# Kernel optimization log

Measured on AMD Instinct MI355X. Metric: run time of the kernel, lower is better.

## Reference

```python
import jax, jax.numpy as jnp
import numpy as np

P, T, S, D, V, H, FF, L, BLOCK = 4096, 1024, 4, 2048, 32000, 8, 8192, 2, 16
DH = D // H


def _rms(x, g):
    return x * g * jax.lax.rsqrt(jnp.mean(x * x, axis=-1, keepdims=True) + 1e-6)


def _attn(xq, xkv, mask, Wqkv, Wo):
    q = (xq @ Wqkv[:, :D]).reshape(-1, H, DH)
    k = (xkv @ Wqkv[:, D:2 * D]).reshape(-1, H, DH)
    v = (xkv @ Wqkv[:, 2 * D:]).reshape(-1, H, DH)
    s = jnp.einsum('qhd,khd->hqk', q, k) / jnp.asarray(np.sqrt(DH), q.dtype)
    s = jnp.where(mask[None], s, -1e30)
    p = jax.nn.softmax(s, axis=-1)
    o = jnp.einsum('hqk,khd->qhd', p, v).reshape(-1, D)
    return o @ Wo


def _forward(prefix_input_ids, prefix_batch_ids, prefix_position_ids, input_ids,
             batch_ids, position_ids, tail_gather_indices, labels, num_items_in_batch,
             Wt_embed, Wt_qkv, Wt_o, Wt_m1, Wt_m2, gt_ln1, gt_ln2, gt_lnf,
             Wd_embed, Wd_qkv, Wd_o, Wd_m1, Wd_m2, gd_ln1, gd_ln2, gd_lnf):
    # ---- target causal prefill (frozen, torch.no_grad): batch-aware prefix-causal mask ----
    mask_p = (prefix_batch_ids[:, None] == prefix_batch_ids[None, :]) & \
             (prefix_position_ids[:, None] >= prefix_position_ids[None, :])  # [P,P]
    x = Wt_embed[prefix_input_ids]
    for l in range(L):
        xn = _rms(x, gt_ln1[l])
        x = x + _attn(xn, xn, mask_p, Wt_qkv[l], Wt_o[l])
        x = x + jax.nn.gelu(_rms(x, gt_ln2[l]) @ Wt_m1[l]) @ Wt_m2[l]
    hidden = jax.lax.stop_gradient(x)  # extract_context_feature -> last hidden state [P,D]
    logits_t = jax.lax.stop_gradient(_rms(x, gt_lnf) @ Wt_embed.T)  # [P,V]
    # ---- draft block-sparse mask (flex_mask_mod) ----
    full_b = jnp.concatenate([prefix_batch_ids, batch_ids])
    full_p = jnp.concatenate([prefix_position_ids, position_ids])
    qidx = jnp.arange(T)
    kvidx = jnp.arange(P + T)
    qblk = qidx // BLOCK
    anchor_p = position_ids[qblk * BLOCK]  # position of block anchor token [T]
    batch_match = batch_ids[:, None] == full_b[None, :]
    prefix_vis = (kvidx < P)[None, :] & (anchor_p[:, None] > full_p[None, :])
    tail_blk_match = qblk[:, None] == ((kvidx - P) // BLOCK)[None, :]
    mask_d = batch_match & (prefix_vis | tail_blk_match)  # [T, P+T]
    # ---- draft forward: q = tail noise tokens, kv = [prefix hidden ; tail embeds] ----
    xq = Wd_embed[input_ids]
    xkv = jnp.concatenate([hidden, xq], axis=0)
    y = xq + _attn(_rms(xq, gd_ln1), _rms(xkv, gd_ln1), mask_d, Wd_qkv, Wd_o)
    y = y + jax.nn.gelu(_rms(y, gd_ln2) @ Wd_m1) @ Wd_m2
    logits_d = _rms(y, gd_lnf) @ Wd_embed.T  # [T,V]
    # ---- KD loss: forward KL(teacher || student), masked where labels == -100 ----
    teacher = logits_t[tail_gather_indices]
    lpt = jax.nn.log_softmax(teacher, axis=-1)
    lps = jax.nn.log_softmax(logits_d, axis=-1)
    kl = jnp.sum(jnp.exp(lpt) * (lpt - lps), axis=-1)  # [T]
    loss = jnp.where(labels != -100, kl, 0.0).sum() / num_items_in_batch
    return loss


def setup_inputs() -> dict:
    key = jax.random.key(0)
    ks = jax.random.split(key, 16)
    seq, tail = P // S, T // S  # 1024 prefix tokens / 256 tail tokens per sequence
    prefix_batch_ids = jnp.asarray(np.repeat(np.arange(S), seq), jnp.int32)
    prefix_position_ids = jnp.asarray(np.tile(np.arange(seq), S), jnp.int32)
    batch_ids = jnp.asarray(np.repeat(np.arange(S), tail), jnp.int32)
    position_ids = jnp.asarray(np.tile(seq - tail + np.arange(tail), S), jnp.int32)
    tail_gather_indices = jnp.asarray(
        np.repeat(np.arange(S), tail) * seq + np.tile(seq - tail - 1 + np.arange(tail), S), jnp.int32)
    labels = jax.random.randint(ks[0], (T,), 0, V, dtype=jnp.int32).at[::17].set(-100)
    w = lambda k, shape: (0.02 * jax.random.normal(k, shape)).astype(jnp.float32)
    return {
        'prefix_input_ids': jax.random.randint(ks[1], (P,), 0, V, dtype=jnp.int32),
        'prefix_batch_ids': prefix_batch_ids,
        'prefix_position_ids': prefix_position_ids,
        'input_ids': jax.random.randint(ks[2], (T,), 0, V, dtype=jnp.int32),
        'batch_ids': batch_ids,
        'position_ids': position_ids,
        'tail_gather_indices': tail_gather_indices,
        'labels': labels,
        'num_items_in_batch': 4,
        'Wt_embed': w(ks[3], (V, D)),
        'Wt_qkv': w(ks[4], (L, D, 3 * D)),
        'Wt_o': w(ks[5], (L, D, D)),
        'Wt_m1': w(ks[6], (L, D, FF)),
        'Wt_m2': w(ks[7], (L, FF, D)),
        'gt_ln1': jnp.ones((L, D), jnp.float32),
        'gt_ln2': jnp.ones((L, D), jnp.float32),
        'gt_lnf': jnp.ones((D,), jnp.float32),
        'Wd_embed': w(ks[8], (V, D)),
        'Wd_qkv': w(ks[9], (D, 3 * D)),
        'Wd_o': w(ks[10], (D, D)),
        'Wd_m1': w(ks[11], (D, FF)),
        'Wd_m2': w(ks[12], (FF, D)),
        'gd_ln1': jnp.ones((D,), jnp.float32),
        'gd_ln2': jnp.ones((D,), jnp.float32),
        'gd_lnf': jnp.ones((D,), jnp.float32),
    }


def reference(prefix_input_ids, prefix_batch_ids, prefix_position_ids, input_ids,
              batch_ids, position_ids, tail_gather_indices, labels, num_items_in_batch,
              Wt_embed, Wt_qkv, Wt_o, Wt_m1, Wt_m2, gt_ln1, gt_ln2, gt_lnf,
              Wd_embed, Wd_qkv, Wd_o, Wd_m1, Wd_m2, gd_ln1, gd_ln2, gd_lnf):
    return _forward(prefix_input_ids, prefix_batch_ids, prefix_position_ids, input_ids,
                    batch_ids, position_ids, tail_gather_indices, labels, num_items_in_batch,
                    Wt_embed, Wt_qkv, Wt_o, Wt_m1, Wt_m2, gt_ln1, gt_ln2, gt_lnf,
                    Wd_embed, Wd_qkv, Wd_o, Wd_m1, Wd_m2, gd_ln1, gd_ln2, gd_lnf)
```

## Files before the change

kernel.cpp:

```cpp
#include <hip/hip_runtime.h>
#include <math.h>

#define P_TOK 4096
#define T_TOK 1024
#define KV_TOK 5120
#define DIM 2048
#define VOCAB 32000
#define NHEAD 8
#define DHEAD 256
#define FFDIM 8192
#define NLAYER 2

using f32x4  = __attribute__((ext_vector_type(4))) float;
using bf16x4 = __attribute__((ext_vector_type(4))) __bf16;
using bf16x8 = __attribute__((ext_vector_type(8))) __bf16;

typedef const __attribute__((address_space(1))) void* gp1_t;
typedef __attribute__((address_space(3))) void* lp3_t;

__device__ __forceinline__ void gload16(const void* g, void* l) {
  __builtin_amdgcn_global_load_lds((gp1_t)g, (lp3_t)l, 16, 0, 0);
}

__device__ __forceinline__ unsigned pack_bf2(float a, float b) {
  union { __bf16 h[2]; unsigned u; } x;
  x.h[0] = (__bf16)a; x.h[1] = (__bf16)b; return x.u;
}

__device__ __forceinline__ float gelu_tanh(float u) {
  const float k2 = 1.5957691216057308f * (u + 0.044715f * u * u * u);
  return u / (1.0f + __expf(-k2));
}

template<typename CT, bool ACCUM, int EPI>
__global__ __launch_bounds__(256) void gemm_bt(
    const __bf16* __restrict__ A, const __bf16* __restrict__ B, CT* __restrict__ C,
    int M, int N, int K, int lda, int ldb, int ldc)
{
  __shared__ __align__(16) __bf16 As[2][128][64];
  __shared__ __align__(16) __bf16 Bs[2][128][64];
  const int tid = threadIdx.x;
  const int lane = tid & 63, wave = tid >> 6;

  int bx = blockIdx.x, by = blockIdx.y;
  {
    const int gx = gridDim.x, gy = gridDim.y;
    const int nwg = gx * gy;
    if ((nwg & 7) == 0) {
      const int lin = bx * gy + by;
      const int cpx = nwg >> 3;
      const int swz = (lin & 7) * cpx + (lin >> 3);
      bx = swz / gy; by = swz % gy;
    }
  }
  const int bm = by << 7, bn = bx << 7;

  const int fr = lane & 15, fq = lane >> 4;
  const int wm = (wave >> 1) << 6, wn = (wave & 1) << 6;
  const int l8 = lane >> 3;
  const int c8 = ((lane & 7) ^ l8) << 3;
  const int sw = fr & 7;

  const __bf16* ga[4]; const __bf16* gb[4];
  char* la[4]; char* lb[4];
#pragma unroll
  for (int i = 0; i < 4; ++i) {
    const int c = (wave << 2) + i;
    const int row = (c << 3) + l8;
    ga[i] = A + (size_t)(bm + row) * lda + c8;
    gb[i] = B + (size_t)(bn + row) * ldb + c8;
    la[i] = (char*)(&As[0][0][0]) + (c << 10);
    lb[i] = (char*)(&Bs[0][0][0]) + (c << 10);
  }
  f32x4 acc[4][4] = {};

  const int nk = K >> 6;

#pragma unroll
  for (int i = 0; i < 4; ++i) { gload16(ga[i], la[i]); gload16(gb[i], lb[i]); }
#pragma unroll
  for (int i = 0; i < 4; ++i) { gload16(ga[i] + 64, la[i] + 16384); gload16(gb[i] + 64, lb[i] + 16384); }

  auto step = [&](const int buf, const int t) {
    if (t + 2 < nk) asm volatile("s_waitcnt vmcnt(8)" ::: "memory");
    else            asm volatile("s_waitcnt vmcnt(0)" ::: "memory");
    asm volatile("s_barrier" ::: "memory");
    bf16x8 a[2][4], b[2][4];
#pragma unroll
    for (int ks = 0; ks < 2; ++ks) {
      const int ce = (((ks << 2) + fq) ^ sw) << 3;
#pragma unroll
      for (int i = 0; i < 4; ++i) {
        a[ks][i] = *reinterpret_cast<const bf16x8*>(&As[buf][wm + (i << 4) + fr][ce]);
        b[ks][i] = *reinterpret_cast<const bf16x8*>(&Bs[buf][wn + (i << 4) + fr][ce]);
      }
    }
    asm volatile("s_waitcnt lgkmcnt(0)" ::: "memory");
    asm volatile("s_barrier" ::: "memory");
    if (t + 2 < nk) {
      const int k2 = (t + 2) << 6;
      const int lo = buf << 14;
#pragma unroll
      for (int i = 0; i < 4; ++i) {
        gload16(ga[i] + k2, la[i] + lo);
        gload16(gb[i] + k2, lb[i] + lo);
      }
    }
    __builtin_amdgcn_sched_barrier(0);
#pragma unroll
    for (int ks = 0; ks < 2; ++ks)
#pragma unroll
      for (int mi = 0; mi < 4; ++mi)
#pragma unroll
        for (int ni = 0; ni < 4; ++ni)
          acc[mi][ni] = __builtin_amdgcn_mfma_f32_16x16x32_bf16(a[ks][mi], b[ks][ni], acc[mi][ni], 0, 0, 0);
  };
  for (int t = 0; t < nk; t += 2) { step(0, t); step(1, t + 1); }

#pragma unroll
  for (int mi = 0; mi < 4; ++mi) {
#pragma unroll
    for (int r = 0; r < 4; ++r) {
      const size_t rowi = (size_t)(bm + wm + (mi << 4) + (fq << 2) + r);
      CT* Crow = C + rowi * ldc + bn + wn + fr;
#pragma unroll
      for (int ni = 0; ni < 4; ++ni) {
        float v = acc[mi][ni][r];
        if (EPI == 1) v = gelu_tanh(v);
        if (ACCUM) Crow[ni << 4] += (CT)v;
        else       Crow[ni << 4] = (CT)v;
      }
    }
  }
}

template<int MODE>
__global__ __launch_bounds__(256, 2) void flash_attn(
    const __bf16* __restrict__ Q, int ldq,
    const __bf16* __restrict__ K, int ldk,
    const __bf16* __restrict__ VT, int lenKV,
    __bf16* __restrict__ Oout, int ldo,
    const int* __restrict__ pb, const int* __restrict__ pp,
    const int* __restrict__ tb, const int* __restrict__ tp)
{
  __shared__ __align__(16) char KsB[64 * 512];
  __shared__ __align__(16) char VtsB[256 * 128];
  __shared__ __align__(16) char PsB[64 * 128];
  const int tid = threadIdx.x;
  const int lane = tid & 63, wave = tid >> 6;
  const int fr = lane & 15, fq = lane >> 4;
  const int sw7 = fr & 7;
  const int q0 = blockIdx.x << 6;
  const int h = blockIdx.y;
  const __bf16* Qh = Q + (size_t)h * DHEAD;
  const __bf16* Kh = K + (size_t)h * DHEAD;
  const __bf16* VTh = VT + (size_t)h * DHEAD * lenKV;

  int qb_l, aux_l;
  if (MODE == 0) { qb_l = pb[q0 + lane]; aux_l = pp[q0 + lane]; }
  else           { qb_l = tb[q0 + lane]; aux_l = tp[((q0 + lane) >> 4) << 4]; }
  const int qb0 = __shfl(qb_l, 0);
  const bool uniform = __all(qb_l == qb0);
  int amax = aux_l;
#pragma unroll
  for (int s = 1; s < 64; s <<= 1) amax = max(amax, __shfl_xor(amax, s));

  const int q_s = q0 + (wave << 4) + fr;
  int qb_s, aux_s;
  if (MODE == 0) { qb_s = pb[q_s]; aux_s = pp[q_s]; }
  else           { qb_s = tb[q_s]; aux_s = tp[(q_s >> 4) << 4]; }
  const int qblk_s = q_s >> 4;

  bf16x8 qreg[8];
#pragma unroll
  for (int ds = 0; ds < 8; ++ds)
    qreg[ds] = *reinterpret_cast<const bf16x8*>(
        Qh + (size_t)q_s * ldq + (ds << 5) + (fq << 3));

  f32x4 acc[16] = {};
  float mrun = -1.0e30f, lrun = 0.0f;

  for (int kv0 = 0; kv0 < lenKV; kv0 += 64) {
    bool ok;
    if (MODE == 0) {
      ok = (pb[kv0 + lane] == qb0) && (pp[kv0 + lane] <= amax);
    } else if (kv0 < P_TOK) {
      ok = (pb[kv0 + lane] == qb0) && (pp[kv0 + lane] < amax);
    } else {
      const int kk = kv0 - P_TOK + lane;
      const int kb = kk >> 4;
      ok = (tb[kk] == qb0) && (kb >= (q0 >> 4)) && (kb <= ((q0 + 63) >> 4));
    }
    if (uniform && !__any(ok)) continue;

    __syncthreads();
#pragma unroll
    for (int i = 0; i < 8; ++i) {
      const int s = wave + (i << 2);
      const int cl = (s << 6) + lane;
      {
        const int r = cl >> 5, c = cl & 31;
        gload16(Kh + (size_t)(kv0 + r) * ldk + ((c ^ (r & 7)) << 3), KsB + (s << 10));
      }
      {
        const int rd = cl >> 3, c = cl & 7;
        gload16(VTh + (size_t)rd * lenKV + kv0 + ((c ^ (rd & 7)) << 3), VtsB + (s << 10));
      }
    }
    __syncthreads();

    f32x4 st[4] = {};
#pragma unroll
    for (int ds = 0; ds < 8; ++ds) {
#pragma unroll
      for (int mt = 0; mt < 4; ++mt) {
        const bf16x8 kf = *reinterpret_cast<const bf16x8*>(
            KsB + ((mt << 4) + fr) * 512 + ((((ds << 2) + fq) ^ sw7) << 4));
        st[mt] = __builtin_amdgcn_mfma_f32_16x16x32_bf16(kf, qreg[ds], st[mt], 0, 0, 0);
      }
    }

    float pv[16];
    float tmax = -3.0e38f;
#pragma unroll
    for (int mt = 0; mt < 4; ++mt) {
      const int kbase = kv0 + (mt << 4) + (fq << 2);
      bool vis[4];
      if (MODE == 0) {
        const int4 pbv = *reinterpret_cast<const int4*>(pb + kbase);
        const int4 ppv = *reinterpret_cast<const int4*>(pp + kbase);
        vis[0] = (pbv.x == qb_s) && (aux_s >= ppv.x);
        vis[1] = (pbv.y == qb_s) && (aux_s >= ppv.y);
        vis[2] = (pbv.z == qb_s) && (aux_s >= ppv.z);
        vis[3] = (pbv.w == qb_s) && (aux_s >= ppv.w);
      } else if (kv0 < P_TOK) {
        const int4 pbv = *reinterpret_cast<const int4*>(pb + kbase);
        const int4 ppv = *reinterpret_cast<const int4*>(pp + kbase);
        vis[0] = (pbv.x == qb_s) && (aux_s > ppv.x);
        vis[1] = (pbv.y == qb_s) && (aux_s > ppv.y);
        vis[2] = (pbv.z == qb_s) && (aux_s > ppv.z);
        vis[3] = (pbv.w == qb_s) && (aux_s > ppv.w);
      } else {
        const int4 tbv = *reinterpret_cast<const int4*>(tb + kbase - P_TOK);
        const bool blkok = (((kv0 - P_TOK) >> 4) + mt) == qblk_s;
        vis[0] = (tbv.x == qb_s) && blkok;
        vis[1] = (tbv.y == qb_s) && blkok;
        vis[2] = (tbv.z == qb_s) && blkok;
        vis[3] = (tbv.w == qb_s) && blkok;
      }
#pragma unroll
      for (int r = 0; r < 4; ++r) {
        const float sv = st[mt][r] * 0.0625f;
        const float val = vis[r] ? sv : -1.0e30f;
        pv[(mt << 2) + r] = val;
        tmax = fmaxf(tmax, val);
      }
    }
    tmax = fmaxf(tmax, __shfl_xor(tmax, 16));
    tmax = fmaxf(tmax, __shfl_xor(tmax, 32));

    const float m_old = mrun;
    const bool grow = tmax > m_old + 8.0f;
    const float mnew = grow ? tmax : m_old;
    float tsum = 0.f;
#pragma unroll
    for (int i = 0; i < 16; ++i) { pv[i] = __expf(pv[i] - mnew); tsum += pv[i]; }
    tsum += __shfl_xor(tsum, 16);
    tsum += __shfl_xor(tsum, 32);
    const float fac = __expf(m_old - mnew);
    lrun = lrun * fac + tsum;
    mrun = mnew;

#pragma unroll
    for (int mt = 0; mt < 4; ++mt) {
#pragma unroll
      for (int rp = 0; rp < 4; rp += 2) {
        const unsigned u = pack_bf2(pv[(mt << 2) + rp], pv[(mt << 2) + rp + 1]);
        *reinterpret_cast<unsigned*>(PsB + ((wave << 4) + fr) * 128
            + ((((mt << 1) + (fq >> 1)) ^ sw7) << 4) + ((fq & 1) << 3) + ((rp >> 1) << 2)) = u;
      }
    }

    if (!__all(!grow)) {
#pragma unroll
      for (int r = 0; r < 4; ++r) {
        const float f_r = __shfl(fac, ((lane >> 4) << 2) + r);
#pragma unroll
        for (int dt = 0; dt < 16; ++dt) acc[dt][r] *= f_r;
      }
    }

#pragma unroll
    for (int kk = 0; kk < 2; ++kk) {
      const bf16x8 pa = *reinterpret_cast<const bf16x8*>(
          PsB + ((wave << 4) + fr) * 128 + ((((kk << 2) + fq) ^ sw7) << 4));
#pragma unroll
      for (int dt = 0; dt < 16; ++dt) {
        const bf16x8 vb = *reinterpret_cast<const bf16x8*>(
            VtsB + ((dt << 4) + fr) * 128 + ((((kk << 2) + fq) ^ sw7) << 4));
        acc[dt] = __builtin_amdgcn_mfma_f32_16x16x32_bf16(pa, vb, acc[dt], 0, 0, 0);
      }
    }
  }

#pragma unroll
  for (int r = 0; r < 4; ++r) {
    const float linv = 1.0f / __shfl(lrun, ((lane >> 4) << 2) + r);
    const int rowg = q0 + (wave << 4) + (fq << 2) + r;
#pragma unroll
    for (int dt = 0; dt < 16; ++dt)
      Oout[(size_t)rowg * ldo + (size_t)h * DHEAD + (dt << 4) + fr] = (__bf16)(acc[dt][r] * linv);
  }
}

__global__ __launch_bounds__(256) void transpose_set(
    const float* __restrict__ sQkv, const float* __restrict__ sO,
    const float* __restrict__ sM1, const float* __restrict__ sM2,
    __bf16* __restrict__ dstBase)
{
  int b = blockIdx.x;
  const float* src; long doff; int R, Cc;
  if (b < 12288)      { src = sQkv; R = DIM;   Cc = 3 * DIM; doff = 0; }
  else if (b < 16384) { b -= 12288; src = sO;  R = DIM; Cc = DIM;
                        doff = (long)3 * DIM * DIM; }
  else if (b < 32768) { b -= 16384; src = sM1; R = DIM; Cc = FFDIM;
                        doff = (long)3 * DIM * DIM + (long)DIM * DIM; }
  else                { b -= 32768; src = sM2; R = FFDIM; Cc = DIM;
                        doff = (long)3 * DIM * DIM + (long)DIM * DIM + (long)DIM * FFDIM; }
  __bf16* dst = dstBase + doff;
  const int tilesX = Cc >> 5;
  const int bx = (b % tilesX) << 5, by = (b / tilesX) << 5;
  __shared__ float tile[32][33];
  const int tx = threadIdx.x & 31, ty = threadIdx.x >> 5;
#pragma unroll
  for (int k = 0; k < 32; k += 8)
    tile[ty + k][tx] = src[(size_t)(by + ty + k) * Cc + bx + tx];
  __syncthreads();
#pragma unroll
  for (int k = 0; k < 32; k += 8)
    dst[(size_t)(bx + ty + k) * R + by + tx] = (__bf16)tile[tx][ty + k];
}

__global__ __launch_bounds__(256) void conv_bf16(const float* __restrict__ src,
    __bf16* __restrict__ dst, long n8)
{
  const long i = (long)blockIdx.x * 256 + threadIdx.x;
  if (i >= n8) return;
  const float4 a = reinterpret_cast<const float4*>(src)[i * 2];
  const float4 b = reinterpret_cast<const float4*>(src)[i * 2 + 1];
  bf16x8 h;
  h[0] = (__bf16)a.x; h[1] = (__bf16)a.y; h[2] = (__bf16)a.z; h[3] = (__bf16)a.w;
  h[4] = (__bf16)b.x; h[5] = (__bf16)b.y; h[6] = (__bf16)b.z; h[7] = (__bf16)b.w;
  reinterpret_cast<bf16x8*>(dst)[i] = h;
}

__global__ __launch_bounds__(256) void rms_bf16(const float* __restrict__ x,
    const float* __restrict__ g, __bf16* __restrict__ y, const int* __restrict__ row_idx)
{
  __shared__ float red[256];
  const int r = blockIdx.x;
  const int src = row_idx ? row_idx[r] : r;
  const float* xr = x + (size_t)src * DIM;
  __bf16* yr = y + (size_t)r * DIM;
  const int t = threadIdx.x;
  const float4 v0 = *reinterpret_cast<const float4*>(xr + t * 8);
  const float4 v1 = *reinterpret_cast<const float4*>(xr + t * 8 + 4);
  float ss = v0.x * v0.x + v0.y * v0.y + v0.z * v0.z + v0.w * v0.w
           + v1.x * v1.x + v1.y * v1.y + v1.z * v1.z + v1.w * v1.w;
  red[t] = ss; __syncthreads();
  for (int s = 128; s > 0; s >>= 1) { if (t < s) red[t] += red[t + s]; __syncthreads(); }
  const float inv = rsqrtf(red[0] * (1.0f / DIM) + 1e-6f);
  const float4 g0 = *reinterpret_cast<const float4*>(g + t * 8);
  const float4 g1 = *reinterpret_cast<const float4*>(g + t * 8 + 4);
  bf16x8 h;
  h[0] = (__bf16)(v0.x * g0.x * inv); h[1] = (__bf16)(v0.y * g0.y * inv);
  h[2] = (__bf16)(v0.z * g0.z * inv); h[3] = (__bf16)(v0.w * g0.w * inv);
  h[4] = (__bf16)(v1.x * g1.x * inv); h[5] = (__bf16)(v1.y * g1.y * inv);
  h[6] = (__bf16)(v1.z * g1.z * inv); h[7] = (__bf16)(v1.w * g1.w * inv);
  *reinterpret_cast<bf16x8*>(yr + t * 8) = h;
}

__global__ __launch_bounds__(256) void gather_rows_kernel(const float* __restrict__ tab,
    const int* __restrict__ ids, float* __restrict__ out)
{
  const int r = blockIdx.x;
  const float* src = tab + (size_t)ids[r] * DIM;
  float* dst = out + (size_t)r * DIM;
  const int t = threadIdx.x;
  *reinterpret_cast<float4*>(dst + t * 8) = *reinterpret_cast<const float4*>(src + t * 8);
  *reinterpret_cast<float4*>(dst + t * 8 + 4) = *reinterpret_cast<const float4*>(src + t * 8 + 4);
}

__global__ __launch_bounds__(256) void teacher_softmax_kernel(const float* __restrict__ TL,
    __bf16* __restrict__ PT, float* __restrict__ ENT, float* __restrict__ S1)
{
  __shared__ float sm[256], ss[256];
  const int r = blockIdx.x, t = threadIdx.x;
  const float* tl = TL + (size_t)r * VOCAB;
  __bf16* pt = PT + (size_t)r * VOCAB;
  float m = -3.0e38f, s = 0.f;
  for (int v = t; v < VOCAB; v += 256) {
    const float x = tl[v];
    if (x > m) { s = s * expf(m - x) + 1.f; m = x; }
    else       { s += expf(x - m); }
  }
  sm[t] = m; ss[t] = s; __syncthreads();
  for (int st = 128; st > 0; st >>= 1) {
    if (t < st) {
      const float m2 = sm[t + st], s2 = ss[t + st];
      const float M = fmaxf(sm[t], m2);
      ss[t] = ss[t] * expf(sm[t] - M) + s2 * expf(m2 - M);
      sm[t] = M;
    }
    __syncthreads();
  }
  const float Mt = sm[0], Z = ss[0];
  const float invZ = 1.0f / Z, lZ = logf(Z);
  __syncthreads();
  float ent = 0.f, s1 = 0.f;
  for (int v = t; v < VOCAB; v += 256) {
    const float x = tl[v];
    const float p = expf(x - Mt) * invZ;
    const __bf16 pb_ = (__bf16)p;
    pt[v] = pb_;
    const float pf = (float)pb_;
    ent += pf * (x - Mt - lZ);
    s1 += pf;
  }
  sm[t] = ent; ss[t] = s1; __syncthreads();
  for (int st = 128; st > 0; st >>= 1) {
    if (t < st) { sm[t] += sm[t + st]; ss[t] += ss[t + st]; }
    __syncthreads();
  }
  if (t == 0) { ENT[r] = sm[0]; S1[r] = ss[0]; }
}

__global__ __launch_bounds__(256) void kl_loss_kernel(const float* __restrict__ DL,
    const __bf16* __restrict__ PT, const float* __restrict__ ENT, const float* __restrict__ S1,
    const int* __restrict__ labels, const int* __restrict__ nitems, float* __restrict__ out)
{
  __shared__ float sm[256], ss[256], sc[256];
  const int r = blockIdx.x, t = threadIdx.x;
  if (labels[r] == -100) return;
  const float* dl = DL + (size_t)r * VOCAB;
  const __bf16* pt = PT + (size_t)r * VOCAB;
  float m = -3.0e38f, s = 0.f, cross = 0.f;
  for (int v = t; v < VOCAB; v += 256) {
    const float x = dl[v];
    cross += (float)pt[v] * x;
    if (x > m) { s = s * expf(m - x) + 1.f; m = x; }
    else       { s += expf(x - m); }
  }
  sm[t] = m; ss[t] = s; sc[t] = cross; __syncthreads();
  for (int st = 128; st > 0; st >>= 1) {
    if (t < st) {
      const float m2 = sm[t + st], s2 = ss[t + st];
      const float M = fmaxf(sm[t], m2);
      ss[t] = ss[t] * expf(sm[t] - M) + s2 * expf(m2 - M);
      sm[t] = M;
      sc[t] += sc[t + st];
    }
    __syncthreads();
  }
  if (t == 0) {
    const float lses = sm[0] + logf(ss[0]);
    const int raw = nitems[0];
    const float n = (raw > 0 && raw < 1000000) ? (float)raw : __int_as_float(raw);
    const float loss_r = ENT[r] - sc[0] + lses * S1[r];
    atomicAdd(out, loss_r / n);
  }
}

template<typename CT, bool ACCUM, int EPI>
static inline void g128(const __bf16* A, const __bf16* B, CT* C,
                        int M, int N, int K, int lda, int ldb, int ldc, hipStream_t s)
{
  gemm_bt<CT, ACCUM, EPI><<<dim3(N / 128, M / 128), 256, 0, s>>>(A, B, C, M, N, K, lda, ldb, ldc);
}

extern "C" void kernel_launch(void* const* d_in, const int* in_sizes, int n_in,
                              void* d_out, int out_size, void* d_ws, size_t ws_size,
                              hipStream_t stream)
{
  const int* prefix_ids = (const int*)d_in[0];
  const int* pb        = (const int*)d_in[1];
  const int* pp        = (const int*)d_in[2];
  const int* input_ids = (const int*)d_in[3];
  const int* tb        = (const int*)d_in[4];
  const int* tp        = (const int*)d_in[5];
  const int* tgi       = (const int*)d_in[6];
  const int* labels    = (const int*)d_in[7];
  const int* nitems    = (const int*)d_in[8];
  const float* Wt_embed = (const float*)d_in[9];
  const float* Wt_qkv   = (const float*)d_in[10];
  const float* Wt_o     = (const float*)d_in[11];
  const float* Wt_m1    = (const float*)d_in[12];
  const float* Wt_m2    = (const float*)d_in[13];
  const float* gt_ln1   = (const float*)d_in[14];
  const float* gt_ln2   = (const float*)d_in[15];
  const float* gt_lnf   = (const float*)d_in[16];
  const float* Wd_embed = (const float*)d_in[17];
  const float* Wd_qkv   = (const float*)d_in[18];
  const float* Wd_o     = (const float*)d_in[19];
  const float* Wd_m1    = (const float*)d_in[20];
  const float* Wd_m2    = (const float*)d_in[21];
  const float* gd_ln1   = (const float*)d_in[22];
  const float* gd_ln2   = (const float*)d_in[23];
  const float* gd_lnf   = (const float*)d_in[24];

  char* base = (char*)d_ws;
  size_t off = 0;
  auto alloc = [&](size_t bytes) { size_t o = off; off += (bytes + 255) & ~(size_t)255; return o; };
  const size_t oX    = alloc((size_t)P_TOK * DIM * 4);
  const size_t oXNb  = alloc((size_t)KV_TOK * DIM * 2);
  const size_t oQKVb = alloc((size_t)P_TOK * 3 * DIM * 2);
  const size_t oOb   = alloc((size_t)P_TOK * DIM * 2);
  const size_t oVT   = alloc((size_t)DIM * KV_TOK * 2);
  const size_t oMHb  = alloc((size_t)P_TOK * FFDIM * 2);
  const size_t oY    = alloc((size_t)T_TOK * DIM * 4);
  const size_t oPT   = alloc((size_t)T_TOK * VOCAB * 2);
  const size_t oENT  = alloc((size_t)T_TOK * 4);
  const size_t oS1   = alloc((size_t)T_TOK * 4);
  const size_t oEMB  = alloc((size_t)VOCAB * DIM * 2);
  const size_t oWB   = alloc((size_t)(3 * DIM * DIM + DIM * DIM + DIM * FFDIM + FFDIM * DIM) * 2);
  if (ws_size < off) return;

  float*  X    = (float*)(base + oX);
  __bf16* XNb  = (__bf16*)(base + oXNb);
  __bf16* QKVb = (__bf16*)(base + oQKVb);
  __bf16* Ob   = (__bf16*)(base + oOb);
  __bf16* VT   = (__bf16*)(base + oVT);
  __bf16* MHb  = (__bf16*)(base + oMHb);
  float*  Y    = (float*)(base + oY);
  __bf16* PT   = (__bf16*)(base + oPT);
  float*  ENT  = (float*)(base + oENT);
  float*  S1   = (float*)(base + oS1);
  __bf16* embB = (__bf16*)(base + oEMB);
  __bf16* wQkvT = (__bf16*)(base + oWB);
  __bf16* wOT   = wQkvT + (size_t)3 * DIM * DIM;
  __bf16* wM1T  = wOT + (size_t)DIM * DIM;
  __bf16* wM2T  = wM1T + (size_t)FFDIM * DIM;
  float*  TLOG = (float*)(base + oQKVb);
  float*  DLOG = (float*)(base + oQKVb);

  hipMemsetAsync(d_out, 0, sizeof(float), stream);

  gather_rows_kernel<<<P_TOK, 256, 0, stream>>>(Wt_embed, prefix_ids, X);
  for (int l = 0; l < NLAYER; ++l) {
    transpose_set<<<49152, 256, 0, stream>>>(
        Wt_qkv + (size_t)l * DIM * 3 * DIM, Wt_o + (size_t)l * DIM * DIM,
        Wt_m1 + (size_t)l * DIM * FFDIM, Wt_m2 + (size_t)l * FFDIM * DIM, wQkvT);

    rms_bf16<<<P_TOK, 256, 0, stream>>>(X, gt_ln1 + l * DIM, XNb, nullptr);
    g128<__bf16, false, 0>(XNb, wQkvT, QKVb, P_TOK, 2 * DIM, DIM, DIM, DIM, 2 * DIM, stream);
    g128<__bf16, false, 0>(wQkvT + (size_t)2 * DIM * DIM, XNb, VT,
                           DIM, P_TOK, DIM, DIM, DIM, P_TOK, stream);
    flash_attn<0><<<dim3(P_TOK / 64, NHEAD), 256, 0, stream>>>(
        QKVb, 2 * DIM, QKVb + DIM, 2 * DIM, VT, P_TOK, Ob, DIM, pb, pp, nullptr, nullptr);
    g128<float, true, 0>(Ob, wOT, X, P_TOK, DIM, DIM, DIM, DIM, DIM, stream);
    rms_bf16<<<P_TOK, 256, 0, stream>>>(X, gt_ln2 + l * DIM, XNb, nullptr);
    g128<__bf16, false, 1>(XNb, wM1T, MHb, P_TOK, FFDIM, DIM, DIM, DIM, FFDIM, stream);
    g128<float, true, 0>(MHb, wM2T, X, P_TOK, DIM, FFDIM, FFDIM, FFDIM, DIM, stream);
  }

  rms_bf16<<<T_TOK, 256, 0, stream>>>(X, gt_lnf, XNb, tgi);
  conv_bf16<<<((long)VOCAB * DIM / 8 + 255) / 256, 256, 0, stream>>>(Wt_embed, embB, (long)VOCAB * DIM / 8);
  g128<float, false, 0>(XNb, embB, TLOG, T_TOK, VOCAB, DIM, DIM, DIM, VOCAB, stream);
  teacher_softmax_kernel<<<T_TOK, 256, 0, stream>>>(TLOG, PT, ENT, S1);

  gather_rows_kernel<<<T_TOK, 256, 0, stream>>>(Wd_embed, input_ids, Y);
  transpose_set<<<49152, 256, 0, stream>>>(Wd_qkv, Wd_o, Wd_m1, Wd_m2, wQkvT);

  rms_bf16<<<P_TOK, 256, 0, stream>>>(X, gd_ln1, XNb, nullptr);
  rms_bf16<<<T_TOK, 256, 0, stream>>>(Y, gd_ln1, XNb + (size_t)P_TOK * DIM, nullptr);
  __bf16* Qb = QKVb;
  __bf16* Kb = QKVb + (size_t)T_TOK * DIM;
  g128<__bf16, false, 0>(XNb + (size_t)P_TOK * DIM, wQkvT, Qb, T_TOK, DIM, DIM, DIM, DIM, DIM, stream);
  g128<__bf16, false, 0>(XNb, wQkvT + (size_t)DIM * DIM, Kb, KV_TOK, DIM, DIM, DIM, DIM, DIM, stream);
  g128<__bf16, false, 0>(wQkvT + (size_t)2 * DIM * DIM, XNb, VT,
                         DIM, KV_TOK, DIM, DIM, DIM, KV_TOK, stream);
  flash_attn<1><<<dim3(T_TOK / 64, NHEAD), 256, 0, stream>>>(
      Qb, DIM, Kb, DIM, VT, KV_TOK, Ob, DIM, pb, pp, tb, tp);
  g128<float, true, 0>(Ob, wOT, Y, T_TOK, DIM, DIM, DIM, DIM, DIM, stream);
  rms_bf16<<<T_TOK, 256, 0, stream>>>(Y, gd_ln2, XNb, nullptr);
  g128<__bf16, false, 1>(XNb, wM1T, MHb, T_TOK, FFDIM, DIM, DIM, DIM, FFDIM, stream);
  g128<float, true, 0>(MHb, wM2T, Y, T_TOK, DIM, FFDIM, FFDIM, FFDIM, DIM, stream);
  rms_bf16<<<T_TOK, 256, 0, stream>>>(Y, gd_lnf, XNb, nullptr);
  conv_bf16<<<((long)VOCAB * DIM / 8 + 255) / 256, 256, 0, stream>>>(Wd_embed, embB, (long)VOCAB * DIM / 8);
  g128<float, false, 0>(XNb, embB, DLOG, T_TOK, VOCAB, DIM, DIM, DIM, VOCAB, stream);

  kl_loss_kernel<<<T_TOK, 256, 0, stream>>>(DLOG, PT, ENT, S1, labels, nitems, (float*)d_out);
}
```

Before: 2.487 ms.

## Add 256x256-tile GEMM with XCD-aware block swizzle for large matmuls

Adds a new 512-thread GEMM kernel with 256x256 output tiles, double-buffered LDS staging via global_load_lds, and a block-index remap that groups tiles per XCD. It replaces the 128x128 kernel for the target QKV projection, the target MLP up-projection with GELU, and both vocabulary logit GEMMs. The larger tiles raise arithmetic intensity and cut global and L2 traffic per FLOP. In exchange it uses 128 KB of LDS per block and many accumulator registers, which limits occupancy to one block per CU. It also leaves fewer blocks for the smaller-M logit GEMMs.

```diff
diff --git a/kernel.cpp b/kernel.cpp
--- a/kernel.cpp
+++ b/kernel.cpp
@@ -73,7 +73,6 @@
     lb[i] = (char*)(&Bs[0][0][0]) + (c << 10);
   }
   f32x4 acc[4][4] = {};
-
   const int nk = K >> 6;
 
 #pragma unroll
@@ -123,6 +122,103 @@
     for (int r = 0; r < 4; ++r) {
       const size_t rowi = (size_t)(bm + wm + (mi << 4) + (fq << 2) + r);
       CT* Crow = C + rowi * ldc + bn + wn + fr;
+#pragma unroll
+      for (int ni = 0; ni < 4; ++ni) {
+        float v = acc[mi][ni][r];
+        if (EPI == 1) v = gelu_tanh(v);
+        if (ACCUM) Crow[ni << 4] += (CT)v;
+        else       Crow[ni << 4] = (CT)v;
+      }
+    }
+  }
+}
+
+template<typename CT, bool ACCUM, int EPI>
+__global__ __launch_bounds__(512, 2) void gemm256(
+    const __bf16* __restrict__ A, const __bf16* __restrict__ B, CT* __restrict__ C,
+    int M, int N, int K, int lda, int ldb, int ldc)
+{
+  __shared__ __align__(16) __bf16 As[2][256][64];
+  __shared__ __align__(16) __bf16 Bs[2][256][64];
+  const int tid = threadIdx.x;
+  const int lane = tid & 63, wave = tid >> 6;
+
+  const int nwg = gridDim.x;
+  const int gy = M >> 8;
+  const int q8 = nwg >> 3, r8 = nwg & 7;
+  const int xcd = blockIdx.x & 7, idx = blockIdx.x >> 3;
+  const int swz = (xcd < r8 ? xcd * (q8 + 1) : r8 * (q8 + 1) + (xcd - r8) * q8) + idx;
+  const int bm = (swz % gy) << 8;
+  const int bn = (swz / gy) << 8;
+
+  const int fr = lane & 15, fq = lane >> 4;
+  const int rm = wave >> 2;
+  const int cn = wave & 3;
+  const int l8 = lane >> 3;
+  const int c8 = ((lane & 7) ^ l8) << 3;
+  const int sw = fr & 7;
+
+  const __bf16* ga[4]; const __bf16* gb[4];
+  char* la[4]; char* lb[4];
+#pragma unroll
+  for (int i = 0; i < 4; ++i) {
+    const int row = (i << 6) + (wave << 3) + l8;
+    ga[i] = A + (size_t)(bm + row) * lda + c8;
+    gb[i] = B + (size_t)(bn + row) * ldb + c8;
+    la[i] = (char*)(&As[0][0][0]) + (i << 13) + (wave << 10);
+    lb[i] = (char*)(&Bs[0][0][0]) + (i << 13) + (wave << 10);
+  }
+  f32x4 acc[8][4] = {};
+  const int nk = K >> 6;
+
+#pragma unroll
+  for (int i = 0; i < 4; ++i) { gload16(ga[i], la[i]); gload16(gb[i], lb[i]); }
+#pragma unroll
+  for (int i = 0; i < 4; ++i) { gload16(ga[i] + 64, la[i] + 32768); gload16(gb[i] + 64, lb[i] + 32768); }
+
+  auto step = [&](const int buf, const int t) {
+    if (t + 2 < nk) asm volatile("s_waitcnt vmcnt(8)" ::: "memory");
+    else            asm volatile("s_waitcnt vmcnt(0)" ::: "memory");
+    asm volatile("s_barrier" ::: "memory");
+    bf16x8 a[2][8], b[2][4];
+#pragma unroll
+    for (int ks = 0; ks < 2; ++ks) {
+      const int ce = (((ks << 2) + fq) ^ sw) << 3;
+#pragma unroll
+      for (int i = 0; i < 8; ++i)
+        a[ks][i] = *reinterpret_cast<const bf16x8*>(&As[buf][(rm << 7) + (i << 4) + fr][ce]);
+#pragma unroll
+      for (int i = 0; i < 4; ++i)
+        b[ks][i] = *reinterpret_cast<const bf16x8*>(&Bs[buf][(cn << 6) + (i << 4) + fr][ce]);
+    }
+    asm volatile("s_waitcnt lgkmcnt(0)" ::: "memory");
+    asm volatile("s_barrier" ::: "memory");
+    if (t + 2 < nk) {
+      const int k2 = (t + 2) << 6;
+      const int lo = buf << 15;
+#pragma unroll
+      for (int i = 0; i < 4; ++i) {
+        gload16(ga[i] + k2, la[i] + lo);
+        gload16(gb[i] + k2, lb[i] + lo);
+      }
+    }
+    __builtin_amdgcn_sched_barrier(0);
+#pragma unroll
+    for (int ks = 0; ks < 2; ++ks)
+#pragma unroll
+      for (int mi = 0; mi < 8; ++mi)
+#pragma unroll
+        for (int ni = 0; ni < 4; ++ni)
+          acc[mi][ni] = __builtin_amdgcn_mfma_f32_16x16x32_bf16(a[ks][mi], b[ks][ni], acc[mi][ni], 0, 0, 0);
+  };
+  for (int t = 0; t < nk; t += 2) { step(0, t); step(1, t + 1); }
+
+#pragma unroll
+  for (int mi = 0; mi < 8; ++mi) {
+#pragma unroll
+    for (int r = 0; r < 4; ++r) {
+      const size_t rowi = (size_t)(bm + (rm << 7) + (mi << 4) + (fq << 2) + r);
+      CT* Crow = C + rowi * ldc + bn + (cn << 6) + fr;
 #pragma unroll
       for (int ni = 0; ni < 4; ++ni) {
         float v = acc[mi][ni][r];
@@ -476,6 +572,12 @@
                         int M, int N, int K, int lda, int ldb, int ldc, hipStream_t s)
 {
   gemm_bt<CT, ACCUM, EPI><<<dim3(N / 128, M / 128), 256, 0, s>>>(A, B, C, M, N, K, lda, ldb, ldc);
+}
+template<typename CT, bool ACCUM, int EPI>
+static inline void g256(const __bf16* A, const __bf16* B, CT* C,
+                        int M, int N, int K, int lda, int ldb, int ldc, hipStream_t s)
+{
+  gemm256<CT, ACCUM, EPI><<<dim3((M >> 8) * (N >> 8)), 512, 0, s>>>(A, B, C, M, N, K, lda, ldb, ldc);
 }
 
 extern "C" void kernel_launch(void* const* d_in, const int* in_sizes, int n_in,
@@ -552,20 +654,20 @@
         Wt_m1 + (size_t)l * DIM * FFDIM, Wt_m2 + (size_t)l * FFDIM * DIM, wQkvT);
 
     rms_bf16<<<P_TOK, 256, 0, stream>>>(X, gt_ln1 + l * DIM, XNb, nullptr);
-    g128<__bf16, false, 0>(XNb, wQkvT, QKVb, P_TOK, 2 * DIM, DIM, DIM, DIM, 2 * DIM, stream);
+    g256<__bf16, false, 0>(XNb, wQkvT, QKVb, P_TOK, 2 * DIM, DIM, DIM, DIM, 2 * DIM, stream);
     g128<__bf16, false, 0>(wQkvT + (size_t)2 * DIM * DIM, XNb, VT,
                            DIM, P_TOK, DIM, DIM, DIM, P_TOK, stream);
     flash_attn<0><<<dim3(P_TOK / 64, NHEAD), 256, 0, stream>>>(
         QKVb, 2 * DIM, QKVb + DIM, 2 * DIM, VT, P_TOK, Ob, DIM, pb, pp, nullptr, nullptr);
     g128<float, true, 0>(Ob, wOT, X, P_TOK, DIM, DIM, DIM, DIM, DIM, stream);
     rms_bf16<<<P_TOK, 256, 0, stream>>>(X, gt_ln2 + l * DIM, XNb, nullptr);
-    g128<__bf16, false, 1>(XNb, wM1T, MHb, P_TOK, FFDIM, DIM, DIM, DIM, FFDIM, stream);
+    g256<__bf16, false, 1>(XNb, wM1T, MHb, P_TOK, FFDIM, DIM, DIM, DIM, FFDIM, stream);
     g128<float, true, 0>(MHb, wM2T, X, P_TOK, DIM, FFDIM, FFDIM, FFDIM, DIM, stream);
   }
 
   rms_bf16<<<T_TOK, 256, 0, stream>>>(X, gt_lnf, XNb, tgi);
   conv_bf16<<<((long)VOCAB * DIM / 8 + 255) / 256, 256, 0, stream>>>(Wt_embed, embB, (long)VOCAB * DIM / 8);
-  g128<float, false, 0>(XNb, embB, TLOG, T_TOK, VOCAB, DIM, DIM, DIM, VOCAB, stream);
+  g256<float, false, 0>(XNb, embB, TLOG, T_TOK, VOCAB, DIM, DIM, DIM, VOCAB, stream);
   teacher_softmax_kernel<<<T_TOK, 256, 0, stream>>>(TLOG, PT, ENT, S1);
 
   gather_rows_kernel<<<T_TOK, 256, 0, stream>>>(Wd_embed, input_ids, Y);
@@ -587,7 +689,7 @@
   g128<float, true, 0>(MHb, wM2T, Y, T_TOK, DIM, FFDIM, FFDIM, FFDIM, DIM, stream);
   rms_bf16<<<T_TOK, 256, 0, stream>>>(Y, gd_lnf, XNb, nullptr);
   conv_bf16<<<((long)VOCAB * DIM / 8 + 255) / 256, 256, 0, stream>>>(Wd_embed, embB, (long)VOCAB * DIM / 8);
-  g128<float, false, 0>(XNb, embB, DLOG, T_TOK, VOCAB, DIM, DIM, DIM, VOCAB, stream);
+  g256<float, false, 0>(XNb, embB, DLOG, T_TOK, VOCAB, DIM, DIM, DIM, VOCAB, stream);
 
   kl_loss_kernel<<<T_TOK, 256, 0, stream>>>(DLOG, PT, ENT, S1, labels, nitems, (float*)d_out);
 }
```

Measured after the change: 2.981 ms. +19.8%, slower.
